# Kernel optimization log

Measured on AMD Instinct MI355X. Metric: run time of the kernel, lower is better.

## Reference

```python
import jax, jax.numpy as jnp
import numpy as np

N = 100000
E = 1600000
IN_DIM = 128
OUT_DIM = 128
H = 4
HD = OUT_DIM // H  # 32
NEG_SLOPE = 0.2
EPS_SOFTMAX = 1e-8
EPS_LN = 1e-5


def setup_inputs() -> dict:
    key = jax.random.key(0)
    ks = jax.random.split(key, 6)
    h = jax.random.normal(ks[0], (N, IN_DIM), dtype=jnp.float32)
    edge_index = jax.random.randint(ks[1], (2, E), 0, N, dtype=jnp.int32)
    W = jax.random.normal(ks[2], (IN_DIM, OUT_DIM), dtype=jnp.float32) / np.sqrt(IN_DIM)
    W_self = jax.random.normal(ks[3], (IN_DIM, OUT_DIM), dtype=jnp.float32) / np.sqrt(IN_DIM)
    a_in = jax.random.normal(ks[4], (H, 2 * HD), dtype=jnp.float32) * 0.01
    a_out = jax.random.normal(ks[5], (H, 2 * HD), dtype=jnp.float32) * 0.01
    bias = jnp.zeros((OUT_DIM,), dtype=jnp.float32)
    ln_gamma = jnp.ones((OUT_DIM,), dtype=jnp.float32)
    ln_beta = jnp.zeros((OUT_DIM,), dtype=jnp.float32)
    return {"h": h, "edge_index": edge_index, "W": W, "W_self": W_self,
            "a_in": a_in, "a_out": a_out, "bias": bias,
            "ln_gamma": ln_gamma, "ln_beta": ln_beta}


def _attention_aggregate(h_proj, sender, receiver, attn_vec, num_nodes):
    # h_proj: (N, H, HD); sender/receiver: (E,); attn_vec: (H, 2*HD)
    h_sender = h_proj[sender]      # (E, H, HD)
    h_receiver = h_proj[receiver]  # (E, H, HD)
    # e = sum over concat([h_sender, h_receiver]) * attn_vec, split halves
    e = (jnp.einsum('ehd,hd->eh', h_sender, attn_vec[:, :HD])
         + jnp.einsum('ehd,hd->eh', h_receiver, attn_vec[:, HD:]))
    e = jax.nn.leaky_relu(e, NEG_SLOPE)
    e_max = jax.ops.segment_max(e, receiver, num_segments=num_nodes)  # (N, H)
    alpha = jnp.exp(e - e_max[receiver])
    alpha_sum = jax.ops.segment_sum(alpha, receiver, num_segments=num_nodes)
    alpha = alpha / (alpha_sum[receiver] + EPS_SOFTMAX)
    msg = h_sender * alpha[..., None]  # (E, H, HD)
    return jax.ops.segment_sum(msg, receiver, num_segments=num_nodes)  # (N, H, HD)


def reference(h, edge_index, W, W_self, a_in, a_out, bias, ln_gamma, ln_beta):
    n = h.shape[0]
    h_proj = (h @ W).reshape(n, H, HD)
    h_self = h @ W_self
    src, dst = edge_index[0], edge_index[1]
    h_in = _attention_aggregate(h_proj, src, dst, a_in, n)   # 'in' direction
    h_out = _attention_aggregate(h_proj, dst, src, a_out, n)  # 'out' direction
    combined = h_self + h_in.reshape(n, -1) + h_out.reshape(n, -1) + bias
    mean = combined.mean(axis=-1, keepdims=True)
    var = combined.var(axis=-1, keepdims=True)
    normed = (combined - mean) * jax.lax.rsqrt(var + EPS_LN)
    return normed * ln_gamma + ln_beta
```

## Files before the change

kernel.cpp:

```cpp
#include <hip/hip_runtime.h>
#include <math.h>

#define HEADS 4
#define HD 32
#define DIM 128
#define NEG_SLOPE 0.2f
#define EPS_SM 1e-8f
#define EPS_LN 1e-5f
#define GROWS 64
#define SH1 9
#define PB 128

__device__ __forceinline__ float lrelu(float x) { return x > 0.f ? x : NEG_SLOPE * x; }
__device__ __forceinline__ unsigned bf16rne(float x) {
    unsigned b = __float_as_uint(x);
    return (b + 0x7fffu + ((b >> 16) & 1u)) >> 16;
}

template<int LIM> __device__ __forceinline__ void rmax4(float& a, float& b, float& c, float& d) {
#pragma unroll
    for (int s = 1; s < LIM; s <<= 1) {
        a = fmaxf(a, __shfl_xor(a, s, 64));
        b = fmaxf(b, __shfl_xor(b, s, 64));
        c = fmaxf(c, __shfl_xor(c, s, 64));
        d = fmaxf(d, __shfl_xor(d, s, 64));
    }
}
template<int LIM> __device__ __forceinline__ void rsum4(float& a, float& b, float& c, float& d) {
#pragma unroll
    for (int s = 1; s < LIM; s <<= 1) {
        a += __shfl_xor(a, s, 64);
        b += __shfl_xor(b, s, 64);
        c += __shfl_xor(c, s, 64);
        d += __shfl_xor(d, s, 64);
    }
}

__global__ __launch_bounds__(256) void dual_gemm_k(const float* __restrict__ h,
                                                   const float* __restrict__ W,
                                                   const float* __restrict__ V,
                                                   const float* __restrict__ a_in,
                                                   const float* __restrict__ a_out,
                                                   float* __restrict__ h_self,
                                                   unsigned* __restrict__ hp_pk,
                                                   float* __restrict__ pA0, float* __restrict__ pA1,
                                                   float* __restrict__ pB0, float* __restrict__ pB1,
                                                   int N) {
    __shared__ float As[32][GROWS];
    __shared__ float Ws[32][DIM];
    __shared__ float Vs[32][DIM];
    __shared__ float ainL[256], aoutL[256];
    const int tid = threadIdx.x;
    const int cg = tid & 15;
    const int rg = tid >> 4;
    const int row0 = blockIdx.x * GROWS;

    ainL[tid] = a_in[tid];
    aoutL[tid] = a_out[tid];

    float accP[4][8], accS[4][8];
#pragma unroll
    for (int r = 0; r < 4; ++r)
#pragma unroll
        for (int c = 0; c < 8; ++c) { accP[r][c] = 0.f; accS[r][c] = 0.f; }

    for (int kc = 0; kc < 4; ++kc) {
        __syncthreads();
#pragma unroll
        for (int p = 0; p < 2; ++p) {
            int f = tid + p * 256;
            int r = f >> 3, c4 = f & 7;
            float4 v = make_float4(0.f, 0.f, 0.f, 0.f);
            if (row0 + r < N) v = ((const float4*)h)[(size_t)(row0 + r) * 32 + kc * 8 + c4];
            As[c4 * 4 + 0][r] = v.x;
            As[c4 * 4 + 1][r] = v.y;
            As[c4 * 4 + 2][r] = v.z;
            As[c4 * 4 + 3][r] = v.w;
        }
#pragma unroll
        for (int p = 0; p < 4; ++p) {
            int f = tid + p * 256;
            int lk = f >> 5, c4 = f & 31;
            ((float4*)&Ws[lk][0])[c4] = ((const float4*)W)[(size_t)(kc * 32 + lk) * 32 + c4];
            ((float4*)&Vs[lk][0])[c4] = ((const float4*)V)[(size_t)(kc * 32 + lk) * 32 + c4];
        }
        __syncthreads();
#pragma unroll
        for (int kk = 0; kk < 32; ++kk) {
            float4 a = *(const float4*)&As[kk][rg * 4];
            float4 w0 = *(const float4*)&Ws[kk][cg * 8];
            float4 w1 = *(const float4*)&Ws[kk][cg * 8 + 4];
            float4 v0 = *(const float4*)&Vs[kk][cg * 8];
            float4 v1 = *(const float4*)&Vs[kk][cg * 8 + 4];
            float av[4] = {a.x, a.y, a.z, a.w};
            float wv[8] = {w0.x, w0.y, w0.z, w0.w, w1.x, w1.y, w1.z, w1.w};
            float vv[8] = {v0.x, v0.y, v0.z, v0.w, v1.x, v1.y, v1.z, v1.w};
#pragma unroll
            for (int r = 0; r < 4; ++r)
#pragma unroll
                for (int c = 0; c < 8; ++c) {
                    accP[r][c] += av[r] * wv[c];
                    accS[r][c] += av[r] * vv[c];
                }
        }
    }

#pragma unroll
    for (int r = 0; r < 4; ++r) {
        int row = row0 + rg * 4 + r;
        if (row < N) {
            float4 s0 = make_float4(accS[r][0], accS[r][1], accS[r][2], accS[r][3]);
            float4 s1 = make_float4(accS[r][4], accS[r][5], accS[r][6], accS[r][7]);
            ((float4*)h_self)[(size_t)row * 32 + cg * 2] = s0;
            ((float4*)h_self)[(size_t)row * 32 + cg * 2 + 1] = s1;
        }
    }

    const int head = cg >> 2, qi = cg & 3;
#pragma unroll
    for (int r = 0; r < 4; ++r) {
        float d0 = 0.f, d1 = 0.f, d2 = 0.f, d3 = 0.f;
#pragma unroll
        for (int c = 0; c < 8; ++c) {
            float v = accP[r][c];
            int k = head * 64 + qi * 8 + c;
            d0 += v * ainL[k];
            d1 += v * ainL[k + 32];
            d2 += v * aoutL[k];
            d3 += v * aoutL[k + 32];
        }
        d0 += __shfl_xor(d0, 1, 64); d0 += __shfl_xor(d0, 2, 64);
        d1 += __shfl_xor(d1, 1, 64); d1 += __shfl_xor(d1, 2, 64);
        d2 += __shfl_xor(d2, 1, 64); d2 += __shfl_xor(d2, 2, 64);
        d3 += __shfl_xor(d3, 1, 64); d3 += __shfl_xor(d3, 2, 64);
        if (qi == 0) {
            int row = row0 + rg * 4 + r;
            if (row < N) {
                pA0[row * 4 + head] = d0;
                pA1[row * 4 + head] = d1;
                pB0[row * 4 + head] = d2;
                pB1[row * 4 + head] = d3;
            }
        }
    }

    __syncthreads();
    float* lds2 = &Ws[0][0];
    if (cg >= 8) {
#pragma unroll
        for (int r = 0; r < 4; ++r) {
            int rl = rg * 4 + r;
#pragma unroll
            for (int c = 0; c < 8; ++c) lds2[rl * 64 + (cg - 8) * 8 + c] = accP[r][c];
        }
    }
    __syncthreads();
    if (cg < 8) {
#pragma unroll
        for (int r = 0; r < 4; ++r) {
            int rl = rg * 4 + r;
            int row = row0 + rl;
            if (row < N) {
                unsigned pks[8];
#pragma unroll
                for (int c = 0; c < 8; ++c)
                    pks[c] = bf16rne(accP[r][c]) | (bf16rne(lds2[rl * 64 + cg * 8 + c]) << 16);
                uint4* dst = (uint4*)(hp_pk + (size_t)row * 64 + cg * 8);
                dst[0] = make_uint4(pks[0], pks[1], pks[2], pks[3]);
                dst[1] = make_uint4(pks[4], pks[5], pks[6], pks[7]);
            }
        }
    }
}

__global__ __launch_bounds__(256) void part1a_k(const int* __restrict__ ei, int* __restrict__ cntmat,
                                                int E, int N, int NBIN) {
    __shared__ int lcnt[512];
    const int t = threadIdx.x;
    const int CH = (E + gridDim.x - 1) / gridDim.x;
    const int e0 = blockIdx.x * CH;
    const int e1 = min(e0 + CH, E);
    for (int i = t; i < 512; i += 256) lcnt[i] = 0;
    __syncthreads();
    for (int e = e0 + t; e < e1; e += 256) {
        int s = ei[e], d = ei[E + e];
        atomicAdd(&lcnt[d >> SH1], 1);
        atomicAdd(&lcnt[(N + s) >> SH1], 1);
    }
    __syncthreads();
    for (int i = t; i < NBIN; i += 256) cntmat[i * PB + blockIdx.x] = lcnt[i];
}

__global__ __launch_bounds__(128) void scanB_k(const int* __restrict__ cntmat,
                                               int* __restrict__ blkoff, int* __restrict__ btot) {
    __shared__ int ls[PB];
    const int bin = blockIdx.x;
    const int t = threadIdx.x;
    int v = cntmat[bin * PB + t];
    ls[t] = v;
    __syncthreads();
#pragma unroll
    for (int d = 1; d < PB; d <<= 1) {
        int u = (t >= d) ? ls[t - d] : 0;
        __syncthreads();
        ls[t] += u;
        __syncthreads();
    }
    blkoff[bin * PB + t] = ls[t] - v;
    if (t == PB - 1) btot[bin] = ls[t];
}

__global__ __launch_bounds__(256) void scanC_k(const int* __restrict__ btot,
                                               int* __restrict__ bbase, int NBIN, int twoE) {
    __shared__ int ls[256];
    int t = threadIdx.x;
    int i0 = 2 * t, i1 = 2 * t + 1;
    int v0 = (i0 < NBIN) ? btot[i0] : 0;
    int v1 = (i1 < NBIN) ? btot[i1] : 0;
    int pair = v0 + v1;
    ls[t] = pair;
    __syncthreads();
#pragma unroll
    for (int d = 1; d < 256; d <<= 1) {
        int u = (t >= d) ? ls[t - d] : 0;
        __syncthreads();
        ls[t] += u;
        __syncthreads();
    }
    int excl = ls[t] - pair;
    if (i0 < NBIN) bbase[i0] = excl;
    if (i1 < NBIN) bbase[i1] = excl + v0;
    if (t == 0) bbase[NBIN] = twoE;
}

__global__ __launch_bounds__(256) void part1b_k(const int* __restrict__ ei,
                                                const int* __restrict__ bbase,
                                                const int* __restrict__ blkoff,
                                                unsigned* __restrict__ rec, int E, int N, int NBIN) {
    __shared__ int gb[512];
    __shared__ int lcur[512];
    const int t = threadIdx.x;
    const int CH = (E + gridDim.x - 1) / gridDim.x;
    const int e0 = blockIdx.x * CH;
    const int e1 = min(e0 + CH, E);
    for (int i = t; i < 512; i += 256) lcur[i] = 0;
    for (int i = t; i < NBIN; i += 256) gb[i] = bbase[i] + blkoff[i * PB + blockIdx.x];
    __syncthreads();
    for (int e = e0 + t; e < e1; e += 256) {
        int s = ei[e], d = ei[E + e];
        int b1 = d >> SH1;
        int r1 = atomicAdd(&lcur[b1], 1);
        rec[gb[b1] + r1] = (unsigned)s | ((unsigned)(d & 511) << 20);
        int so = N + s;
        int b2 = so >> SH1;
        int r2 = atomicAdd(&lcur[b2], 1);
        rec[gb[b2] + r2] = (unsigned)d | ((unsigned)(so & 511) << 20);
    }
}

__global__ __launch_bounds__(256) void build2_k(const unsigned* __restrict__ rec,
                                                const int* __restrict__ bbase,
                                                int* __restrict__ off, int* __restrict__ csr,
                                                int M, int twoE, int NBIN) {
    __shared__ int lcnt[512];
    __shared__ int lcur[512];
    __shared__ int ls[256];
    const int b = blockIdx.x;
    const int t = threadIdx.x;
    const int base = bbase[b];
    const int cnt = bbase[b + 1] - base;
    const int seg0 = b << SH1;
    for (int i = t; i < 512; i += 256) lcnt[i] = 0;
    __syncthreads();
    for (int k = t; k < cnt; k += 256) atomicAdd(&lcnt[rec[base + k] >> 20], 1);
    __syncthreads();
    int v0 = lcnt[2 * t], v1 = lcnt[2 * t + 1];
    int pair = v0 + v1;
    ls[t] = pair;
    __syncthreads();
#pragma unroll
    for (int d = 1; d < 256; d <<= 1) {
        int u = (t >= d) ? ls[t - d] : 0;
        __syncthreads();
        ls[t] += u;
        __syncthreads();
    }
    int excl = ls[t] - pair;
    lcur[2 * t] = excl;
    lcur[2 * t + 1] = excl + v0;
    int sg = seg0 + 2 * t;
    if (sg < M) off[sg] = base + excl;
    if (sg + 1 < M) off[sg + 1] = base + excl + v0;
    if (b == NBIN - 1 && t == 0) off[M] = twoE;
    __syncthreads();
    for (int k = t; k < cnt; k += 256) {
        unsigned r = rec[base + k];
        int pos = atomicAdd(&lcur[r >> 20], 1);
        csr[base + pos] = (int)(r & 0xFFFFFu);
    }
}

__global__ __launch_bounds__(256) void node_aggr_ln_k(const unsigned* __restrict__ hp_pk,
                                                      const float* __restrict__ h_self,
                                                      const float* __restrict__ pA0, const float* __restrict__ pA1,
                                                      const float* __restrict__ pB0, const float* __restrict__ pB1,
                                                      const int* __restrict__ off, const int* __restrict__ csr,
                                                      const float* __restrict__ bias,
                                                      const float* __restrict__ gamma,
                                                      const float* __restrict__ beta,
                                                      float* __restrict__ out, int N) {
    __shared__ uint4 lw[4][64];
    const int wave = threadIdx.x >> 6;
    const int lane = threadIdx.x & 63;
    const int n = blockIdx.x * 4 + wave;
    if (n >= N) return;
    const int l15 = lane & 15;
    const int q = lane >> 4;
    const unsigned lwoff = (unsigned)((q << 4) + ((l15 >> 3) << 3));
    const char* lwbase = (const char*)&lw[wave][0];
    const uint4* __restrict__ hpp4 = (const uint4*)hp_pk;

    float alo0 = 0.f, alo1 = 0.f, alo2 = 0.f, alo3 = 0.f;
    float ahi0 = 0.f, ahi1 = 0.f, ahi2 = 0.f, ahi3 = 0.f;

#pragma unroll
    for (int dir = 0; dir < 2; ++dir) {
        const int seg = (dir == 0) ? n : N + n;
        const int beg = off[seg], end = off[seg + 1];
        const int len = end - beg;
        if (len == 0) continue;
        const float* __restrict__ p0 = (dir == 0) ? pA0 : pB0;
        const float* __restrict__ p1 = (dir == 0) ? pA1 : pB1;
        float4 r1 = ((const float4*)p1)[n];

        if (len <= 64) {
            int sid = 0;
            float e0 = -INFINITY, e1 = -INFINITY, e2 = -INFINITY, e3 = -INFINITY;
            if (lane < len) {
                sid = csr[beg + lane];
                float4 r0 = ((const float4*)p0)[sid];
                e0 = lrelu(r0.x + r1.x);
                e1 = lrelu(r0.y + r1.y);
                e2 = lrelu(r0.z + r1.z);
                e3 = lrelu(r0.w + r1.w);
            }
            float m0 = e0, m1 = e1, m2 = e2, m3 = e3;
            if (len <= 16)      rmax4<16>(m0, m1, m2, m3);
            else if (len <= 32) rmax4<32>(m0, m1, m2, m3);
            else                rmax4<64>(m0, m1, m2, m3);
            float w0 = 0.f, w1 = 0.f, w2 = 0.f, w3 = 0.f;
            if (lane < len) {
                w0 = expf(e0 - m0); w1 = expf(e1 - m1);
                w2 = expf(e2 - m2); w3 = expf(e3 - m3);
            }
            float s0 = w0, s1 = w1, s2 = w2, s3 = w3;
            if (len <= 16)      rsum4<16>(s0, s1, s2, s3);
            else if (len <= 32) rsum4<32>(s0, s1, s2, s3);
            else                rsum4<64>(s0, s1, s2, s3);
            w0 *= 1.f / (s0 + EPS_SM);
            w1 *= 1.f / (s1 + EPS_SM);
            w2 *= 1.f / (s2 + EPS_SM);
            w3 *= 1.f / (s3 + EPS_SM);
            unsigned pkA = bf16rne(w0) | (bf16rne(w2) << 16);
            unsigned pkB = bf16rne(w1) | (bf16rne(w3) << 16);
            lw[wave][lane] = make_uint4(pkA, (unsigned)sid, pkB, (unsigned)sid);
            const int nt = (len + 3) >> 2;
#pragma unroll 2
            for (int t = 0; t < nt; ++t) {
                uint2 wv = *(const uint2*)(lwbase + t * 64 + lwoff);
                uint4 v = hpp4[((size_t)wv.y << 4) + l15];
                float wa = __uint_as_float(wv.x << 16);
                float wb = __uint_as_float(wv.x & 0xffff0000u);
                alo0 += wa * __uint_as_float(v.x << 16);
                ahi0 += wb * __uint_as_float(v.x & 0xffff0000u);
                alo1 += wa * __uint_as_float(v.y << 16);
                ahi1 += wb * __uint_as_float(v.y & 0xffff0000u);
                alo2 += wa * __uint_as_float(v.z << 16);
                ahi2 += wb * __uint_as_float(v.z & 0xffff0000u);
                alo3 += wa * __uint_as_float(v.w << 16);
                ahi3 += wb * __uint_as_float(v.w & 0xffff0000u);
            }
        } else {
            float m0 = -INFINITY, m1 = -INFINITY, m2 = -INFINITY, m3 = -INFINITY;
            for (int base = beg; base < end; base += 64) {
                int j = base + lane;
                if (j < end) {
                    int sid = csr[j];
                    float4 r0 = ((const float4*)p0)[sid];
                    m0 = fmaxf(m0, lrelu(r0.x + r1.x));
                    m1 = fmaxf(m1, lrelu(r0.y + r1.y));
                    m2 = fmaxf(m2, lrelu(r0.z + r1.z));
                    m3 = fmaxf(m3, lrelu(r0.w + r1.w));
                }
            }
            rmax4<64>(m0, m1, m2, m3);
            float s0 = 0.f, s1 = 0.f, s2 = 0.f, s3 = 0.f;
            for (int base = beg; base < end; base += 64) {
                int j = base + lane;
                if (j < end) {
                    int sid = csr[j];
                    float4 r0 = ((const float4*)p0)[sid];
                    s0 += expf(lrelu(r0.x + r1.x) - m0);
                    s1 += expf(lrelu(r0.y + r1.y) - m1);
                    s2 += expf(lrelu(r0.z + r1.z) - m2);
                    s3 += expf(lrelu(r0.w + r1.w) - m3);
                }
            }
            rsum4<64>(s0, s1, s2, s3);
            const float is0 = 1.f / (s0 + EPS_SM);
            const float is1 = 1.f / (s1 + EPS_SM);
            const float is2 = 1.f / (s2 + EPS_SM);
            const float is3 = 1.f / (s3 + EPS_SM);
            for (int base = beg; base < end; base += 64) {
                int cnt = min(64, end - base);
                int sid = 0;
                float w0 = 0.f, w1 = 0.f, w2 = 0.f, w3 = 0.f;
                if (lane < cnt) {
                    sid = csr[base + lane];
                    float4 r0 = ((const float4*)p0)[sid];
                    w0 = expf(lrelu(r0.x + r1.x) - m0) * is0;
                    w1 = expf(lrelu(r0.y + r1.y) - m1) * is1;
                    w2 = expf(lrelu(r0.z + r1.z) - m2) * is2;
                    w3 = expf(lrelu(r0.w + r1.w) - m3) * is3;
                }
                unsigned pkA = bf16rne(w0) | (bf16rne(w2) << 16);
                unsigned pkB = bf16rne(w1) | (bf16rne(w3) << 16);
                lw[wave][lane] = make_uint4(pkA, (unsigned)sid, pkB, (unsigned)sid);
                const int nt = (cnt + 3) >> 2;
#pragma unroll 2
                for (int t = 0; t < nt; ++t) {
                    uint2 wv = *(const uint2*)(lwbase + t * 64 + lwoff);
                    uint4 v = hpp4[((size_t)wv.y << 4) + l15];
                    float wa = __uint_as_float(wv.x << 16);
                    float wb = __uint_as_float(wv.x & 0xffff0000u);
                    alo0 += wa * __uint_as_float(v.x << 16);
                    ahi0 += wb * __uint_as_float(v.x & 0xffff0000u);
                    alo1 += wa * __uint_as_float(v.y << 16);
                    ahi1 += wb * __uint_as_float(v.y & 0xffff0000u);
                    alo2 += wa * __uint_as_float(v.z << 16);
                    ahi2 += wb * __uint_as_float(v.z & 0xffff0000u);
                    alo3 += wa * __uint_as_float(v.w << 16);
                    ahi3 += wb * __uint_as_float(v.w & 0xffff0000u);
                }
            }
        }
    }

#pragma unroll
    for (int s = 16; s < 64; s <<= 1) {
        alo0 += __shfl_xor(alo0, s, 64); alo1 += __shfl_xor(alo1, s, 64);
        alo2 += __shfl_xor(alo2, s, 64); alo3 += __shfl_xor(alo3, s, 64);
        ahi0 += __shfl_xor(ahi0, s, 64); ahi1 += __shfl_xor(ahi1, s, 64);
        ahi2 += __shfl_xor(ahi2, s, 64); ahi3 += __shfl_xor(ahi3, s, 64);
    }

    size_t bb = (size_t)n * DIM;
    float4 hs0 = *(const float4*)(h_self + bb + 4 * l15);
    float4 hs1 = *(const float4*)(h_self + bb + 64 + 4 * l15);
    float4 b0 = *(const float4*)(bias + 4 * l15);
    float4 b1 = *(const float4*)(bias + 64 + 4 * l15);
    float x0 = hs0.x + alo0 + b0.x;
    float x1 = hs0.y + alo1 + b0.y;
    float x2 = hs0.z + alo2 + b0.z;
    float x3 = hs0.w + alo3 + b0.w;
    float y0 = hs1.x + ahi0 + b1.x;
    float y1 = hs1.y + ahi1 + b1.y;
    float y2 = hs1.z + ahi2 + b1.z;
    float y3 = hs1.w + ahi3 + b1.w;
    float sum = x0 + x1 + x2 + x3 + y0 + y1 + y2 + y3;
    float sq = x0 * x0 + x1 * x1 + x2 * x2 + x3 * x3
             + y0 * y0 + y1 * y1 + y2 * y2 + y3 * y3;
#pragma unroll
    for (int m = 1; m < 64; m <<= 1) {
        sum += __shfl_xor(sum, m, 64);
        sq += __shfl_xor(sq, m, 64);
    }
    float mean = sum * (1.f / 512.f);
    float var = sq * (1.f / 512.f) - mean * mean;
    float inv = rsqrtf(var + EPS_LN);
    if (lane < 16) {
        float4 g0 = *(const float4*)(gamma + 4 * l15);
        float4 g1 = *(const float4*)(gamma + 64 + 4 * l15);
        float4 be0 = *(const float4*)(beta + 4 * l15);
        float4 be1 = *(const float4*)(beta + 64 + 4 * l15);
        float4 o0 = make_float4((x0 - mean) * inv * g0.x + be0.x,
                                (x1 - mean) * inv * g0.y + be0.y,
                                (x2 - mean) * inv * g0.z + be0.z,
                                (x3 - mean) * inv * g0.w + be0.w);
        float4 o1 = make_float4((y0 - mean) * inv * g1.x + be1.x,
                                (y1 - mean) * inv * g1.y + be1.y,
                                (y2 - mean) * inv * g1.z + be1.z,
                                (y3 - mean) * inv * g1.w + be1.w);
        *(float4*)(out + bb + 4 * l15) = o0;
        *(float4*)(out + bb + 64 + 4 * l15) = o1;
    }
}

extern "C" void kernel_launch(void* const* d_in, const int* in_sizes, int n_in,
                              void* d_out, int out_size, void* d_ws, size_t ws_size,
                              hipStream_t stream) {
    const float* h      = (const float*)d_in[0];
    const int*   ei     = (const int*)d_in[1];
    const float* W      = (const float*)d_in[2];
    const float* W_self = (const float*)d_in[3];
    const float* a_in   = (const float*)d_in[4];
    const float* a_out  = (const float*)d_in[5];
    const float* bias   = (const float*)d_in[6];
    const float* gamma  = (const float*)d_in[7];
    const float* beta   = (const float*)d_in[8];
    float* out = (float*)d_out;

    const int N = in_sizes[0] / DIM;
    const int E = in_sizes[1] / 2;
    const int M = 2 * N;
    const int NBIN = (M + (1 << SH1) - 1) >> SH1;
    const int twoE = 2 * E;

    float* ws = (float*)d_ws;
    size_t off_f = 0;
    float* h_self = ws + off_f; off_f += (size_t)N * DIM;
    unsigned* hp_pk = (unsigned*)(ws + off_f); off_f += (size_t)N * 64;
    float* pA0 = ws + off_f; off_f += (size_t)N * 4;
    float* pA1 = ws + off_f; off_f += (size_t)N * 4;
    float* pB0 = ws + off_f; off_f += (size_t)N * 4;
    float* pB1 = ws + off_f; off_f += (size_t)N * 4;
    int* ip = (int*)(ws + off_f);
    size_t off_i = 0;
    int* cntmat = ip + off_i; off_i += (size_t)NBIN * PB;
    int* blkoff = ip + off_i; off_i += (size_t)NBIN * PB;
    int* btot   = ip + off_i; off_i += NBIN;
    int* bbase  = ip + off_i; off_i += (size_t)NBIN + 1;
    int* off    = ip + off_i; off_i += (size_t)M + 1;
    unsigned* rec = (unsigned*)(ip + off_i); off_i += (size_t)twoE;
    int* csr    = ip + off_i; off_i += (size_t)twoE;

    part1a_k<<<PB, 256, 0, stream>>>(ei, cntmat, E, N, NBIN);
    scanB_k<<<NBIN, PB, 0, stream>>>(cntmat, blkoff, btot);
    scanC_k<<<1, 256, 0, stream>>>(btot, bbase, NBIN, twoE);
    part1b_k<<<PB, 256, 0, stream>>>(ei, bbase, blkoff, rec, E, N, NBIN);
    build2_k<<<NBIN, 256, 0, stream>>>(rec, bbase, off, csr, M, twoE, NBIN);

    dual_gemm_k<<<(N + GROWS - 1) / GROWS, 256, 0, stream>>>(h, W, W_self, a_in, a_out,
                                                             h_self, hp_pk, pA0, pA1, pB0, pB1, N);

    node_aggr_ln_k<<<(N + 3) / 4, 256, 0, stream>>>(hp_pk, h_self, pA0, pA1, pB0, pB1,
                                                    off, csr, bias, gamma, beta, out, N);
}
```

Measured before the change: 458.6 us.

## Switch gathered features to fp16 with packed dot2 accumulation and natural layout

The projection kernel now writes fp16 pairs of adjacent columns straight to global memory using cvt_pkrtz. This removes the LDS staging and the two barriers that interleaved the low and high halves as bf16. The aggregation kernel processes two edges per lane group per iteration, permutes the halves together and accumulates with v_dot2_f32_f16. That halves the FMA count and doubles the edges handled per loop trip, and the exact expf calls become __expf. Precision changes from bf16 to fp16 with round-toward-zero, and the layout change requires every consumer of hp_pk to agree.

```diff
diff --git a/kernel.cpp b/kernel.cpp
--- a/kernel.cpp
+++ b/kernel.cpp
@@ -11,10 +11,14 @@
 #define SH1 9
 #define PB 128
 
+typedef _Float16 h2_t __attribute__((ext_vector_type(2)));
+
 __device__ __forceinline__ float lrelu(float x) { return x > 0.f ? x : NEG_SLOPE * x; }
-__device__ __forceinline__ unsigned bf16rne(float x) {
-    unsigned b = __float_as_uint(x);
-    return (b + 0x7fffu + ((b >> 16) & 1u)) >> 16;
+__device__ __forceinline__ unsigned pkh(float a, float b) {
+    return __builtin_bit_cast(unsigned, __builtin_amdgcn_cvt_pkrtz(a, b));
+}
+__device__ __forceinline__ float dot2(unsigned a, unsigned b, float c) {
+    return __builtin_amdgcn_fdot2(__builtin_bit_cast(h2_t, a), __builtin_bit_cast(h2_t, b), c, false);
 }
 
 template<int LIM> __device__ __forceinline__ void rmax4(float& a, float& b, float& c, float& d) {
@@ -144,31 +148,16 @@
         }
     }
 
-    __syncthreads();
-    float* lds2 = &Ws[0][0];
-    if (cg >= 8) {
-#pragma unroll
-        for (int r = 0; r < 4; ++r) {
-            int rl = rg * 4 + r;
-#pragma unroll
-            for (int c = 0; c < 8; ++c) lds2[rl * 64 + (cg - 8) * 8 + c] = accP[r][c];
-        }
-    }
-    __syncthreads();
-    if (cg < 8) {
-#pragma unroll
-        for (int r = 0; r < 4; ++r) {
-            int rl = rg * 4 + r;
-            int row = row0 + rl;
-            if (row < N) {
-                unsigned pks[8];
-#pragma unroll
-                for (int c = 0; c < 8; ++c)
-                    pks[c] = bf16rne(accP[r][c]) | (bf16rne(lds2[rl * 64 + cg * 8 + c]) << 16);
-                uint4* dst = (uint4*)(hp_pk + (size_t)row * 64 + cg * 8);
-                dst[0] = make_uint4(pks[0], pks[1], pks[2], pks[3]);
-                dst[1] = make_uint4(pks[4], pks[5], pks[6], pks[7]);
-            }
+#pragma unroll
+    for (int r = 0; r < 4; ++r) {
+        int row = row0 + rg * 4 + r;
+        if (row < N) {
+            uint4 pk;
+            pk.x = pkh(accP[r][0], accP[r][1]);
+            pk.y = pkh(accP[r][2], accP[r][3]);
+            pk.z = pkh(accP[r][4], accP[r][5]);
+            pk.w = pkh(accP[r][6], accP[r][7]);
+            ((uint4*)hp_pk)[(size_t)row * 16 + cg] = pk;
         }
     }
 }
@@ -309,19 +298,24 @@
                                                       const float* __restrict__ gamma,
                                                       const float* __restrict__ beta,
                                                       float* __restrict__ out, int N) {
-    __shared__ uint4 lw[4][64];
+    __shared__ int sds[4][64];
+    __shared__ uint2 wts[4][64];
     const int wave = threadIdx.x >> 6;
     const int lane = threadIdx.x & 63;
     const int n = blockIdx.x * 4 + wave;
     if (n >= N) return;
     const int l15 = lane & 15;
     const int q = lane >> 4;
-    const unsigned lwoff = (unsigned)((q << 4) + ((l15 >> 3) << 3));
-    const char* lwbase = (const char*)&lw[wave][0];
-    const uint4* __restrict__ hpp4 = (const uint4*)hp_pk;
-
-    float alo0 = 0.f, alo1 = 0.f, alo2 = 0.f, alo3 = 0.f;
-    float ahi0 = 0.f, ahi1 = 0.f, ahi2 = 0.f, ahi3 = 0.f;
+    const unsigned wsel = (l15 & 4) ? 0x07060302u : 0x05040100u;
+    const bool hlo = (l15 < 8);
+    int* sdw = sds[wave];
+    uint2* wtw = wts[wave];
+    const char* hpb = (const char*)hp_pk;
+    const unsigned rowoff = (unsigned)l15 << 4;
+
+    float acc[8];
+#pragma unroll
+    for (int k = 0; k < 8; ++k) acc[k] = 0.f;
 
 #pragma unroll
     for (int dir = 0; dir < 2; ++dir) {
@@ -350,8 +344,8 @@
             else                rmax4<64>(m0, m1, m2, m3);
             float w0 = 0.f, w1 = 0.f, w2 = 0.f, w3 = 0.f;
             if (lane < len) {
-                w0 = expf(e0 - m0); w1 = expf(e1 - m1);
-                w2 = expf(e2 - m2); w3 = expf(e3 - m3);
+                w0 = __expf(e0 - m0); w1 = __expf(e1 - m1);
+                w2 = __expf(e2 - m2); w3 = __expf(e3 - m3);
             }
             float s0 = w0, s1 = w1, s2 = w2, s3 = w3;
             if (len <= 16)      rsum4<16>(s0, s1, s2, s3);
@@ -361,24 +355,27 @@
             w1 *= 1.f / (s1 + EPS_SM);
             w2 *= 1.f / (s2 + EPS_SM);
             w3 *= 1.f / (s3 + EPS_SM);
-            unsigned pkA = bf16rne(w0) | (bf16rne(w2) << 16);
-            unsigned pkB = bf16rne(w1) | (bf16rne(w3) << 16);
-            lw[wave][lane] = make_uint4(pkA, (unsigned)sid, pkB, (unsigned)sid);
-            const int nt = (len + 3) >> 2;
+            sdw[lane] = sid;
+            wtw[lane] = make_uint2(pkh(w0, w1), pkh(w2, w3));
+            const int npair = (len + 7) >> 3;
 #pragma unroll 2
-            for (int t = 0; t < nt; ++t) {
-                uint2 wv = *(const uint2*)(lwbase + t * 64 + lwoff);
-                uint4 v = hpp4[((size_t)wv.y << 4) + l15];
-                float wa = __uint_as_float(wv.x << 16);
-                float wb = __uint_as_float(wv.x & 0xffff0000u);
-                alo0 += wa * __uint_as_float(v.x << 16);
-                ahi0 += wb * __uint_as_float(v.x & 0xffff0000u);
-                alo1 += wa * __uint_as_float(v.y << 16);
-                ahi1 += wb * __uint_as_float(v.y & 0xffff0000u);
-                alo2 += wa * __uint_as_float(v.z << 16);
-                ahi2 += wb * __uint_as_float(v.z & 0xffff0000u);
-                alo3 += wa * __uint_as_float(v.w << 16);
-                ahi3 += wb * __uint_as_float(v.w & 0xffff0000u);
+            for (int t = 0; t < npair; ++t) {
+                int pi = 4 * t + q;
+                uint2 sp = *(const uint2*)&sdw[2 * pi];
+                uint4 wp = *(const uint4*)&wtw[2 * pi];
+                uint4 u = *(const uint4*)(hpb + (((unsigned)sp.x << 8) + rowoff));
+                uint4 v = *(const uint4*)(hpb + (((unsigned)sp.y << 8) + rowoff));
+                unsigned wA = hlo ? wp.x : wp.y;
+                unsigned wB = hlo ? wp.z : wp.w;
+                unsigned wpk = __builtin_amdgcn_perm(wB, wA, wsel);
+                acc[0] = dot2(__builtin_amdgcn_perm(v.x, u.x, 0x05040100u), wpk, acc[0]);
+                acc[1] = dot2(__builtin_amdgcn_perm(v.x, u.x, 0x07060302u), wpk, acc[1]);
+                acc[2] = dot2(__builtin_amdgcn_perm(v.y, u.y, 0x05040100u), wpk, acc[2]);
+                acc[3] = dot2(__builtin_amdgcn_perm(v.y, u.y, 0x07060302u), wpk, acc[3]);
+                acc[4] = dot2(__builtin_amdgcn_perm(v.z, u.z, 0x05040100u), wpk, acc[4]);
+                acc[5] = dot2(__builtin_amdgcn_perm(v.z, u.z, 0x07060302u), wpk, acc[5]);
+                acc[6] = dot2(__builtin_amdgcn_perm(v.w, u.w, 0x05040100u), wpk, acc[6]);
+                acc[7] = dot2(__builtin_amdgcn_perm(v.w, u.w, 0x07060302u), wpk, acc[7]);
             }
         } else {
             float m0 = -INFINITY, m1 = -INFINITY, m2 = -INFINITY, m3 = -INFINITY;
@@ -400,10 +397,10 @@
                 if (j < end) {
                     int sid = csr[j];
                     float4 r0 = ((const float4*)p0)[sid];
-                    s0 += expf(lrelu(r0.x + r1.x) - m0);
-                    s1 += expf(lrelu(r0.y + r1.y) - m1);
-                    s2 += expf(lrelu(r0.z + r1.z) - m2);
-                    s3 += expf(lrelu(r0.w + r1.w) - m3);
+                    s0 += __expf(lrelu(r0.x + r1.x) - m0);
+                    s1 += __expf(lrelu(r0.y + r1.y) - m1);
+                    s2 += __expf(lrelu(r0.z + r1.z) - m2);
+                    s3 += __expf(lrelu(r0.w + r1.w) - m3);
                 }
             }
             rsum4<64>(s0, s1, s2, s3);
@@ -418,29 +415,32 @@
                 if (lane < cnt) {
                     sid = csr[base + lane];
                     float4 r0 = ((const float4*)p0)[sid];
-                    w0 = expf(lrelu(r0.x + r1.x) - m0) * is0;
-                    w1 = expf(lrelu(r0.y + r1.y) - m1) * is1;
-                    w2 = expf(lrelu(r0.z + r1.z) - m2) * is2;
-                    w3 = expf(lrelu(r0.w + r1.w) - m3) * is3;
+                    w0 = __expf(lrelu(r0.x + r1.x) - m0) * is0;
+                    w1 = __expf(lrelu(r0.y + r1.y) - m1) * is1;
+                    w2 = __expf(lrelu(r0.z + r1.z) - m2) * is2;
+                    w3 = __expf(lrelu(r0.w + r1.w) - m3) * is3;
                 }
-                unsigned pkA = bf16rne(w0) | (bf16rne(w2) << 16);
-                unsigned pkB = bf16rne(w1) | (bf16rne(w3) << 16);
-                lw[wave][lane] = make_uint4(pkA, (unsigned)sid, pkB, (unsigned)sid);
-                const int nt = (cnt + 3) >> 2;
+                sdw[lane] = sid;
+                wtw[lane] = make_uint2(pkh(w0, w1), pkh(w2, w3));
+                const int npair = (cnt + 7) >> 3;
 #pragma unroll 2
-                for (int t = 0; t < nt; ++t) {
-                    uint2 wv = *(const uint2*)(lwbase + t * 64 + lwoff);
-                    uint4 v = hpp4[((size_t)wv.y << 4) + l15];
-                    float wa = __uint_as_float(wv.x << 16);
-                    float wb = __uint_as_float(wv.x & 0xffff0000u);
-                    alo0 += wa * __uint_as_float(v.x << 16);
-                    ahi0 += wb * __uint_as_float(v.x & 0xffff0000u);
-                    alo1 += wa * __uint_as_float(v.y << 16);
-                    ahi1 += wb * __uint_as_float(v.y & 0xffff0000u);
-                    alo2 += wa * __uint_as_float(v.z << 16);
-                    ahi2 += wb * __uint_as_float(v.z & 0xffff0000u);
-                    alo3 += wa * __uint_as_float(v.w << 16);
-                    ahi3 += wb * __uint_as_float(v.w & 0xffff0000u);
+                for (int t = 0; t < npair; ++t) {
+                    int pi = 4 * t + q;
+                    uint2 sp = *(const uint2*)&sdw[2 * pi];
+                    uint4 wp = *(const uint4*)&wtw[2 * pi];
+                    uint4 u = *(const uint4*)(hpb + (((unsigned)sp.x << 8) + rowoff));
+                    uint4 v = *(const uint4*)(hpb + (((unsigned)sp.y << 8) + rowoff));
+                    unsigned wA = hlo ? wp.x : wp.y;
+                    unsigned wB = hlo ? wp.z : wp.w;
+                    unsigned wpk = __builtin_amdgcn_perm(wB, wA, wsel);
+                    acc[0] = dot2(__builtin_amdgcn_perm(v.x, u.x, 0x05040100u), wpk, acc[0]);
+                    acc[1] = dot2(__builtin_amdgcn_perm(v.x, u.x, 0x07060302u), wpk, acc[1]);
+                    acc[2] = dot2(__builtin_amdgcn_perm(v.y, u.y, 0x05040100u), wpk, acc[2]);
+                    acc[3] = dot2(__builtin_amdgcn_perm(v.y, u.y, 0x07060302u), wpk, acc[3]);
+                    acc[4] = dot2(__builtin_amdgcn_perm(v.z, u.z, 0x05040100u), wpk, acc[4]);
+                    acc[5] = dot2(__builtin_amdgcn_perm(v.z, u.z, 0x07060302u), wpk, acc[5]);
+                    acc[6] = dot2(__builtin_amdgcn_perm(v.w, u.w, 0x05040100u), wpk, acc[6]);
+                    acc[7] = dot2(__builtin_amdgcn_perm(v.w, u.w, 0x07060302u), wpk, acc[7]);
                 }
             }
         }
@@ -448,25 +448,23 @@
 
 #pragma unroll
     for (int s = 16; s < 64; s <<= 1) {
-        alo0 += __shfl_xor(alo0, s, 64); alo1 += __shfl_xor(alo1, s, 64);
-        alo2 += __shfl_xor(alo2, s, 64); alo3 += __shfl_xor(alo3, s, 64);
-        ahi0 += __shfl_xor(ahi0, s, 64); ahi1 += __shfl_xor(ahi1, s, 64);
-        ahi2 += __shfl_xor(ahi2, s, 64); ahi3 += __shfl_xor(ahi3, s, 64);
+#pragma unroll
+        for (int k = 0; k < 8; ++k) acc[k] += __shfl_xor(acc[k], s, 64);
     }
 
     size_t bb = (size_t)n * DIM;
-    float4 hs0 = *(const float4*)(h_self + bb + 4 * l15);
-    float4 hs1 = *(const float4*)(h_self + bb + 64 + 4 * l15);
-    float4 b0 = *(const float4*)(bias + 4 * l15);
-    float4 b1 = *(const float4*)(bias + 64 + 4 * l15);
-    float x0 = hs0.x + alo0 + b0.x;
-    float x1 = hs0.y + alo1 + b0.y;
-    float x2 = hs0.z + alo2 + b0.z;
-    float x3 = hs0.w + alo3 + b0.w;
-    float y0 = hs1.x + ahi0 + b1.x;
-    float y1 = hs1.y + ahi1 + b1.y;
-    float y2 = hs1.z + ahi2 + b1.z;
-    float y3 = hs1.w + ahi3 + b1.w;
+    float4 hs0 = ((const float4*)(h_self + bb))[2 * l15];
+    float4 hs1 = ((const float4*)(h_self + bb))[2 * l15 + 1];
+    float4 b0 = ((const float4*)bias)[2 * l15];
+    float4 b1 = ((const float4*)bias)[2 * l15 + 1];
+    float x0 = hs0.x + acc[0] + b0.x;
+    float x1 = hs0.y + acc[1] + b0.y;
+    float x2 = hs0.z + acc[2] + b0.z;
+    float x3 = hs0.w + acc[3] + b0.w;
+    float y0 = hs1.x + acc[4] + b1.x;
+    float y1 = hs1.y + acc[5] + b1.y;
+    float y2 = hs1.z + acc[6] + b1.z;
+    float y3 = hs1.w + acc[7] + b1.w;
     float sum = x0 + x1 + x2 + x3 + y0 + y1 + y2 + y3;
     float sq = x0 * x0 + x1 * x1 + x2 * x2 + x3 * x3
              + y0 * y0 + y1 * y1 + y2 * y2 + y3 * y3;
@@ -479,10 +477,10 @@
     float var = sq * (1.f / 512.f) - mean * mean;
     float inv = rsqrtf(var + EPS_LN);
     if (lane < 16) {
-        float4 g0 = *(const float4*)(gamma + 4 * l15);
-        float4 g1 = *(const float4*)(gamma + 64 + 4 * l15);
-        float4 be0 = *(const float4*)(beta + 4 * l15);
-        float4 be1 = *(const float4*)(beta + 64 + 4 * l15);
+        float4 g0 = ((const float4*)gamma)[2 * l15];
+        float4 g1 = ((const float4*)gamma)[2 * l15 + 1];
+        float4 be0 = ((const float4*)beta)[2 * l15];
+        float4 be1 = ((const float4*)beta)[2 * l15 + 1];
         float4 o0 = make_float4((x0 - mean) * inv * g0.x + be0.x,
                                 (x1 - mean) * inv * g0.y + be0.y,
                                 (x2 - mean) * inv * g0.z + be0.z,
@@ -491,8 +489,8 @@
                                 (y1 - mean) * inv * g1.y + be1.y,
                                 (y2 - mean) * inv * g1.z + be1.z,
                                 (y3 - mean) * inv * g1.w + be1.w);
-        *(float4*)(out + bb + 4 * l15) = o0;
-        *(float4*)(out + bb + 64 + 4 * l15) = o1;
+        ((float4*)(out + bb))[2 * l15] = o0;
+        ((float4*)(out + bb))[2 * l15 + 1] = o1;
     }
 }
 
```

New measurement: 454.6 us. About the same (-0.9%).
